# Optimization experiments

Hardware: AMD Instinct MI355X
Metric: run time of the kernel (lower is better)

## Reference

```python
import jax, jax.numpy as jnp
import numpy as np

DECAY = 0.5  # fixed decay constant from the module


def _decay_scan(x):
    """Linear recurrence y_i = DECAY * y_{i-1} + x_i along axis 1, as a
    log-depth associative scan. x: [B, S, H]."""
    a = jnp.full_like(x, DECAY)

    def combine(c1, c2):
        a1, b1 = c1
        a2, b2 = c2
        return (a1 * a2, a2 * b1 + b2)

    _, y = jax.lax.associative_scan(combine, (a, x), axis=1)
    return y


def setup_inputs() -> dict:
    key = jax.random.key(0)
    batch = jax.random.normal(key, (16, 2048, 1024), dtype=jnp.float32)
    return {"batch": batch}


def reference(batch) -> jnp.ndarray:
    # Forward-in-time decay aggregate: fwd[i] = sum_{k<=i} d^{i-k} x[k]
    fwd = _decay_scan(batch)
    # Backward-in-time decay aggregate: bwd[i] = sum_{k>=i} d^{k-i} x[k]
    bwd = jnp.flip(_decay_scan(jnp.flip(batch, axis=1)), axis=1)
    S = batch.shape[1]
    k = jnp.arange(S, dtype=batch.dtype)
    # closed-form geometric sum: n[i] = sum_{j=0}^{i} d^j = (1 - d^{i+1}) / (1 - d)
    n_fwd = (1.0 - DECAY ** (k + 1.0)) / (1.0 - DECAY)
    norm = n_fwd + n_fwd[::-1]  # [S]; note word i is counted in both passes
    return (fwd + bwd) / norm[None, :, None]
```

## Files before the change

### kernel.cpp

```cpp
#include <hip/hip_runtime.h>
#include <stdint.h>


constexpr int B = 16;
constexpr int S = 2048;
constexpr int HV = 256;
constexpr int C = 64;
constexpr int W = 4;
constexpr int NT = C / W;
constexpr int THREADS = 256;
constexpr int NCHUNK = S / C;
constexpr int NBLK = B * NCHUNK;
constexpr int NXCD = 8;

typedef float v4f __attribute__((ext_vector_type(4)));

__device__ __forceinline__ void gload16(const v4f* g, v4f* l) {
    __builtin_amdgcn_global_load_lds(
        (const __attribute__((address_space(1))) uint32_t*)g,
        (__attribute__((address_space(3))) uint32_t*)l, 16, 0, 0);
}

__device__ __forceinline__ void stage(const v4f* xb, int row0,
                                      v4f (*buf)[HV], int w, int lane) {
    int g = row0 + w;
    g = g < 0 ? 0 : (g > S - 1 ? S - 1 : g);
    const v4f* src = xb + (size_t)g * HV + lane;
#pragma unroll
    for (int j = 0; j < 4; ++j) gload16(src + j * 64, &buf[w][j * 64]);
}

__global__ __launch_bounds__(THREADS, 2) void decay_kernel(
    const v4f* __restrict__ x, v4f* __restrict__ out) {
    __shared__ v4f lds[4][W][HV];

    const int bid = blockIdx.x;
    const int swz = (bid & (NXCD - 1)) * (NBLK / NXCD) + (bid >> 3);
    const int cc = swz & (NCHUNK - 1);
    const int b = swz / NCHUNK;
    const int s0 = cc * C;
    const bool edge = (cc == 0) | (cc == NCHUNK - 1);

    const int tid = threadIdx.x;
    const int w = tid >> 6;
    const int lane = tid & 63;
    const v4f* __restrict__ xb = x + (size_t)b * S * HV;
    v4f* __restrict__ ob = out + (size_t)b * S * HV + tid;

    stage(xb, s0 - 8, lds[2], w, lane);
    stage(xb, s0 - 4, lds[3], w, lane);
    stage(xb, s0, lds[0], w, lane);
    stage(xb, s0 + 4, lds[1], w, lane);
    asm volatile("s_waitcnt vmcnt(8)" ::: "memory");
    __builtin_amdgcn_s_barrier();

    v4f facc = (v4f)0.0f;
    if (cc > 0) {
#pragma unroll
        for (int r = 0; r < W; ++r) facc = 0.5f * facc + lds[2][r][tid];
#pragma unroll
        for (int r = 0; r < W; ++r) facc = 0.5f * facc + lds[3][r][tid];
    }
    asm volatile("s_waitcnt lgkmcnt(0)" ::: "memory");
    __builtin_amdgcn_sched_barrier(0);
    __builtin_amdgcn_s_barrier();
    stage(xb, s0 + 8, lds[2], w, lane);

    for (int m = 0; m < NT; ++m) {
        if (m == 0)
            asm volatile("s_waitcnt vmcnt(0)" ::: "memory");
        else
            asm volatile("s_waitcnt vmcnt(4)" ::: "memory");
        __builtin_amdgcn_s_barrier();

        if (m + 3 <= NT + 1)
            stage(xb, s0 + (m + 3) * W, lds[(m + 3) & 3], w, lane);

        const v4f fprev = facc;
        v4f f[W];
#pragma unroll
        for (int r = 0; r < W; ++r) {
            facc = 0.5f * facc + lds[m & 3][r][tid];
            f[r] = facc;
        }

        v4f bacc = (v4f)0.0f;
        const int la0 = s0 + (m + 1) * W;
#pragma unroll
        for (int j = 2 * W - 1; j >= 0; --j) {
            v4f t = (j < W) ? lds[(m + 1) & 3][j][tid]
                            : lds[(m + 2) & 3][j - W][tid];
            if (la0 + j >= S) t = (v4f)0.0f;
            bacc = 0.5f * bacc + t;
        }

#pragma unroll
        for (int r = W - 1; r >= 0; --r) {
            const v4f fr = f[r];
            const v4f fm_ = r ? f[r - 1] : fprev;
            bacc = 0.5f * bacc + (fr - 0.5f * fm_);
            const int i = s0 + m * W + r;
            float rn = 0.25f;
            if (edge)
                rn = 1.0f / (4.0f - exp2f((float)(-i)) -
                             exp2f((float)(i - (S - 1))));
            ob[(size_t)i * HV] = (fr + bacc) * rn;
        }
    }
}

extern "C" void kernel_launch(void* const* d_in, const int* in_sizes, int n_in,
                              void* d_out, int out_size, void* d_ws,
                              size_t ws_size, hipStream_t stream) {
    const v4f* x = (const v4f*)d_in[0];
    v4f* out = (v4f*)d_out;
    decay_kernel<<<dim3(NBLK), THREADS, 0, stream>>>(x, out);
}
```

Baseline: 238.9 us.

## Split hidden dim in halves with float2 lanes, larger chunks and 8-row steps

Each block now covers half of the hidden dimension, with each thread owning a float2 instead of a float4. Chunks grow from 64 to 128 rows and steps from 4 to 8 rows, so the halo recompute per chunk shrinks and the backward lookahead needs only one buffer of 8 rows. The pipeline keeps more loads in flight through templated wait counts, and staging always issues even past the end. The intent is lower halo overhead and more in-flight memory per block, at the cost of narrower per-thread stores and different block counts.

```diff
diff --git a/kernel.cpp b/kernel.cpp
--- a/kernel.cpp
+++ b/kernel.cpp
@@ -4,115 +4,126 @@
 
 constexpr int B = 16;
 constexpr int S = 2048;
-constexpr int HV = 256;
-constexpr int C = 64;
-constexpr int W = 4;
+constexpr int H2 = 512;
+constexpr int BH = 256;
+constexpr int C = 128;
+constexpr int W = 8;
 constexpr int NT = C / W;
 constexpr int THREADS = 256;
 constexpr int NCHUNK = S / C;
-constexpr int NBLK = B * NCHUNK;
+constexpr int NBLK = B * NCHUNK * 2;
 constexpr int NXCD = 8;
 
-typedef float v4f __attribute__((ext_vector_type(4)));
+typedef float v2f __attribute__((ext_vector_type(2)));
 
-__device__ __forceinline__ void gload16(const v4f* g, v4f* l) {
+__device__ __forceinline__ void gload16(const v2f* g, v2f* l) {
     __builtin_amdgcn_global_load_lds(
         (const __attribute__((address_space(1))) uint32_t*)g,
         (__attribute__((address_space(3))) uint32_t*)l, 16, 0, 0);
 }
 
-__device__ __forceinline__ void stage(const v4f* xb, int row0,
-                                      v4f (*buf)[HV], int w, int lane) {
-    int g = row0 + w;
-    g = g < 0 ? 0 : (g > S - 1 ? S - 1 : g);
-    const v4f* src = xb + (size_t)g * HV + lane;
+__device__ __forceinline__ void stage(const v2f* __restrict__ xh, int row0,
+                                      v2f (*buf)[BH], int w, int lane) {
 #pragma unroll
-    for (int j = 0; j < 4; ++j) gload16(src + j * 64, &buf[w][j * 64]);
+    for (int k = 0; k < 2; ++k) {
+        int g = row0 + 2 * w + k;
+        g = g < 0 ? 0 : (g > S - 1 ? S - 1 : g);
+        const v2f* src = xh + (size_t)g * H2 + 2 * lane;
+        gload16(src, &buf[2 * w + k][0]);
+        gload16(src + 128, &buf[2 * w + k][128]);
+    }
+}
+
+template <int VM>
+__device__ __forceinline__ void body(int m, int s0, bool edge,
+                                     const v2f* __restrict__ xh,
+                                     v2f* __restrict__ op, int tid, int w,
+                                     int lane, v2f (*lds)[W][BH], v2f& facc) {
+    if constexpr (VM == 4)
+        asm volatile("s_waitcnt vmcnt(4)" ::: "memory");
+    else if constexpr (VM == 12)
+        asm volatile("s_waitcnt vmcnt(12)" ::: "memory");
+    else
+        asm volatile("s_waitcnt vmcnt(20)" ::: "memory");
+    __builtin_amdgcn_s_barrier();
+
+    stage(xh, s0 + (m + 3) * W, lds[(m + 3) & 3], w, lane);
+
+    const v2f fprev = facc;
+    v2f f[W];
+#pragma unroll
+    for (int r = 0; r < W; ++r) {
+        facc = 0.5f * facc + lds[m & 3][r][tid];
+        f[r] = facc;
+    }
+
+    v2f bacc = (v2f)0.0f;
+    const int la0 = s0 + (m + 1) * W;
+#pragma unroll
+    for (int j = W - 1; j >= 0; --j) {
+        v2f t = lds[(m + 1) & 3][j][tid];
+        if (la0 + j >= S) t = (v2f)0.0f;
+        bacc = 0.5f * bacc + t;
+    }
+
+#pragma unroll
+    for (int r = W - 1; r >= 0; --r) {
+        const v2f fr = f[r];
+        const v2f fm_ = r ? f[r - 1] : fprev;
+        bacc = 0.5f * bacc + (fr - 0.5f * fm_);
+        const int i = s0 + m * W + r;
+        float rn = 0.25f;
+        if (edge)
+            rn = 1.0f / (4.0f - exp2f((float)(-i)) -
+                         exp2f((float)(i - (S - 1))));
+        op[(size_t)i * H2] = (fr + bacc) * rn;
+    }
 }
 
 __global__ __launch_bounds__(THREADS, 2) void decay_kernel(
-    const v4f* __restrict__ x, v4f* __restrict__ out) {
-    __shared__ v4f lds[4][W][HV];
+    const v2f* __restrict__ x, v2f* __restrict__ out) {
+    __shared__ v2f lds[4][W][BH];
 
     const int bid = blockIdx.x;
     const int swz = (bid & (NXCD - 1)) * (NBLK / NXCD) + (bid >> 3);
-    const int cc = swz & (NCHUNK - 1);
-    const int b = swz / NCHUNK;
+    const int h = swz & 1;
+    const int cc = (swz >> 1) & (NCHUNK - 1);
+    const int b = swz >> 5;
     const int s0 = cc * C;
     const bool edge = (cc == 0) | (cc == NCHUNK - 1);
 
     const int tid = threadIdx.x;
     const int w = tid >> 6;
     const int lane = tid & 63;
-    const v4f* __restrict__ xb = x + (size_t)b * S * HV;
-    v4f* __restrict__ ob = out + (size_t)b * S * HV + tid;
+    const v2f* __restrict__ xh = x + (size_t)b * S * H2 + h * BH;
+    v2f* __restrict__ op = out + (size_t)b * S * H2 + h * BH + tid;
 
-    stage(xb, s0 - 8, lds[2], w, lane);
-    stage(xb, s0 - 4, lds[3], w, lane);
-    stage(xb, s0, lds[0], w, lane);
-    stage(xb, s0 + 4, lds[1], w, lane);
-    asm volatile("s_waitcnt vmcnt(8)" ::: "memory");
+    stage(xh, s0 - W, lds[3], w, lane);
+    stage(xh, s0, lds[0], w, lane);
+    stage(xh, s0 + W, lds[1], w, lane);
+    stage(xh, s0 + 2 * W, lds[2], w, lane);
+    asm volatile("s_waitcnt vmcnt(12)" ::: "memory");
     __builtin_amdgcn_s_barrier();
 
-    v4f facc = (v4f)0.0f;
+    v2f facc = (v2f)0.0f;
     if (cc > 0) {
-#pragma unroll
-        for (int r = 0; r < W; ++r) facc = 0.5f * facc + lds[2][r][tid];
 #pragma unroll
         for (int r = 0; r < W; ++r) facc = 0.5f * facc + lds[3][r][tid];
     }
     asm volatile("s_waitcnt lgkmcnt(0)" ::: "memory");
     __builtin_amdgcn_sched_barrier(0);
     __builtin_amdgcn_s_barrier();
-    stage(xb, s0 + 8, lds[2], w, lane);
 
-    for (int m = 0; m < NT; ++m) {
-        if (m == 0)
-            asm volatile("s_waitcnt vmcnt(0)" ::: "memory");
-        else
-            asm volatile("s_waitcnt vmcnt(4)" ::: "memory");
-        __builtin_amdgcn_s_barrier();
-
-        if (m + 3 <= NT + 1)
-            stage(xb, s0 + (m + 3) * W, lds[(m + 3) & 3], w, lane);
-
-        const v4f fprev = facc;
-        v4f f[W];
-#pragma unroll
-        for (int r = 0; r < W; ++r) {
-            facc = 0.5f * facc + lds[m & 3][r][tid];
-            f[r] = facc;
-        }
-
-        v4f bacc = (v4f)0.0f;
-        const int la0 = s0 + (m + 1) * W;
-#pragma unroll
-        for (int j = 2 * W - 1; j >= 0; --j) {
-            v4f t = (j < W) ? lds[(m + 1) & 3][j][tid]
-                            : lds[(m + 2) & 3][j - W][tid];
-            if (la0 + j >= S) t = (v4f)0.0f;
-            bacc = 0.5f * bacc + t;
-        }
-
-#pragma unroll
-        for (int r = W - 1; r >= 0; --r) {
-            const v4f fr = f[r];
-            const v4f fm_ = r ? f[r - 1] : fprev;
-            bacc = 0.5f * bacc + (fr - 0.5f * fm_);
-            const int i = s0 + m * W + r;
-            float rn = 0.25f;
-            if (edge)
-                rn = 1.0f / (4.0f - exp2f((float)(-i)) -
-                             exp2f((float)(i - (S - 1))));
-            ob[(size_t)i * HV] = (fr + bacc) * rn;
-        }
-    }
+    body<4>(0, s0, edge, xh, op, tid, w, lane, lds, facc);
+    body<12>(1, s0, edge, xh, op, tid, w, lane, lds, facc);
+    for (int m = 2; m < NT; ++m)
+        body<20>(m, s0, edge, xh, op, tid, w, lane, lds, facc);
 }
 
 extern "C" void kernel_launch(void* const* d_in, const int* in_sizes, int n_in,
                               void* d_out, int out_size, void* d_ws,
                               size_t ws_size, hipStream_t stream) {
-    const v4f* x = (const v4f*)d_in[0];
-    v4f* out = (v4f*)d_out;
+    const v2f* x = (const v2f*)d_in[0];
+    v2f* out = (v2f*)d_out;
     decay_kernel<<<dim3(NBLK), THREADS, 0, stream>>>(x, out);
 }
```

Result: no change. 240.1 us (+0.5%).
